# Optimization experiments

Measured on AMD Instinct MI355X. Metric: run time of the kernel, lower is better.

## Reference

```python
import jax, jax.numpy as jnp
import numpy as np

B, P, ENC = 64, 196, 512
EMB = ATT = DEC = 256
V = 10000
T = 44


def setup_inputs() -> dict:
    key = jax.random.key(0)
    ks = jax.random.split(key, 16)
    def xavier(k, shape):
        fan_out, fan_in = shape
        std = (2.0 / (fan_in + fan_out)) ** 0.5
        return jax.random.normal(k, shape, dtype=jnp.float32) * std
    return {
        "encoder_out": jax.random.normal(ks[0], (B, P, ENC), dtype=jnp.float32),
        "caption": jax.random.randint(ks[1], (B, T), 0, V),
        "W_enc_att": xavier(ks[2], (ATT, ENC)),
        "W_dec_att": xavier(ks[3], (ATT, DEC)),
        "W_full": xavier(ks[4], (1, ATT)),
        "embedding": jax.random.normal(ks[5], (V, EMB), dtype=jnp.float32) * 0.02,
        "W_init_h": xavier(ks[6], (DEC, ENC)),
        "b_init_h": jnp.zeros((DEC,), dtype=jnp.float32),
        "W_init_c": xavier(ks[7], (DEC, ENC)),
        "b_init_c": jnp.zeros((DEC,), dtype=jnp.float32),
        "W_ih": jax.random.normal(ks[8], (4 * DEC, EMB + ENC), dtype=jnp.float32) * 0.03,
        "b_ih": jnp.zeros((4 * DEC,), dtype=jnp.float32),
        "W_hh": jax.random.normal(ks[9], (4 * DEC, DEC), dtype=jnp.float32) * 0.03,
        "b_hh": jnp.zeros((4 * DEC,), dtype=jnp.float32),
        "W_out": xavier(ks[10], (V, DEC)),
        "b_out": jnp.zeros((V,), dtype=jnp.float32),
    }


def _decoder(encoder_out, caption, W_enc_att, W_dec_att, W_full, embedding,
             W_init_h, b_init_h, W_init_c, b_init_c,
             W_ih, b_ih, W_hh, b_hh, W_out, b_out):
    # embeddings: [B, T, EMB] -> time-major [T, B, EMB]
    emb = embedding[caption].transpose(1, 0, 2)
    # init hidden state from mean pooled encoder features
    avg = encoder_out.mean(axis=1)                      # [B, ENC]
    h0 = avg @ W_init_h.T + b_init_h                    # [B, DEC]
    c0 = avg @ W_init_c.T + b_init_c
    # attention key projection of encoder, constant over time
    att1 = jnp.einsum('bpe,ae->bpa', encoder_out, W_enc_att)  # [B, P, ATT]

    def step(carry, emb_t):
        h, c = carry
        # additive attention
        att2 = h @ W_dec_att.T                          # [B, ATT]
        scores = jnp.einsum('bpa,a->bp',
                            jax.nn.relu(att1 + att2[:, None, :]), W_full[0])
        alpha = jax.nn.softmax(scores, axis=1)          # [B, P]
        ctx = jnp.einsum('bp,bpe->be', alpha, encoder_out)  # [B, ENC]
        # LSTM cell (torch gate order: i, f, g, o)
        x = jnp.concatenate([ctx, emb_t], axis=1)       # [B, ENC+EMB]
        gates = x @ W_ih.T + b_ih + h @ W_hh.T + b_hh   # [B, 4*DEC]
        i, f, g, o = jnp.split(gates, 4, axis=1)
        c_new = jax.nn.sigmoid(f) * c + jax.nn.sigmoid(i) * jnp.tanh(g)
        h_new = jax.nn.sigmoid(o) * jnp.tanh(c_new)
        logits = h_new @ W_out.T + b_out                # [B, V]
        return (h_new, c_new), (logits, alpha)

    # NOTE: torch cat order is [weighted_context, embedding]
    (_, _), (logits, alphas) = jax.lax.scan(step, (h0, c0), emb)
    predictions = logits.transpose(1, 0, 2)             # [B, T, V]
    alphas = alphas.transpose(1, 0, 2)                  # [B, T, P]
    return predictions, alphas


def reference(encoder_out, caption, W_enc_att, W_dec_att, W_full, embedding,
              W_init_h, b_init_h, W_init_c, b_init_c,
              W_ih, b_ih, W_hh, b_hh, W_out, b_out):
    return _decoder(encoder_out, caption, W_enc_att, W_dec_att, W_full, embedding,
                    W_init_h, b_init_h, W_init_c, b_init_c,
                    W_ih, b_ih, W_hh, b_hh, W_out, b_out)
```

## Files before the change

kernel.cpp:

```cpp
#include <hip/hip_runtime.h>

#define B_   64
#define P_   196
#define ENC_ 512
#define ATT_ 256
#define DEC_ 256
#define EMB_ 256
#define V_   10000
#define T_   44
#define G4_  1024
#define XW_  768
#define A1N_ 26624

using short8 = __attribute__((ext_vector_type(8))) short;
using f32x4  = __attribute__((ext_vector_type(4))) float;
typedef _Float16 f16x2 __attribute__((ext_vector_type(2)));

__device__ __forceinline__ unsigned short f2bf(float f) {
    unsigned int u = __float_as_uint(f);
    unsigned int r = (u + 0x7fffu + ((u >> 16) & 1u)) >> 16;
    return (unsigned short)r;
}

__device__ __forceinline__ unsigned int pkh2(float a, float b) {
    f16x2 t; t.x = (_Float16)a; t.y = (_Float16)b;
    return __builtin_bit_cast(unsigned int, t);
}

__device__ __forceinline__ float fdot2f(float wbits, f16x2 xv, float acc) {
    f16x2 wv = __builtin_bit_cast(f16x2, wbits);
#if __has_builtin(__builtin_amdgcn_fdot2)
    return __builtin_amdgcn_fdot2(wv, xv, acc, false);
#else
    acc = fmaf((float)wv.x, (float)xv.x, acc);
    acc = fmaf((float)wv.y, (float)xv.y, acc);
    return acc;
#endif
}
__device__ __forceinline__ float fdot2u(unsigned int wbits, f16x2 xv, float acc) {
    f16x2 wv = __builtin_bit_cast(f16x2, wbits);
#if __has_builtin(__builtin_amdgcn_fdot2)
    return __builtin_amdgcn_fdot2(wv, xv, acc, false);
#else
    acc = fmaf((float)wv.x, (float)xv.x, acc);
    acc = fmaf((float)wv.y, (float)xv.y, acc);
    return acc;
#endif
}

__device__ __forceinline__ void bar() {
    asm volatile("s_waitcnt lgkmcnt(0)" ::: "memory");
    __builtin_amdgcn_s_barrier();
    asm volatile("" ::: "memory");
}

__global__ void k_transpose(const float* __restrict__ src, float* __restrict__ dst,
                            int N, int stride, int off) {
    __shared__ float t[32][33];
    int k0 = blockIdx.x * 32, n0 = blockIdx.y * 32;
    int tx = threadIdx.x & 31, ty = threadIdx.x >> 5;
    for (int r = ty; r < 32; r += 8)
        t[r][tx] = src[(size_t)(n0 + r) * stride + off + k0 + tx];
    __syncthreads();
    for (int r = ty; r < 32; r += 8)
        dst[(size_t)(k0 + r) * N + n0 + tx] = t[tx][r];
}

__global__ __launch_bounds__(256) void k_packWda(const float* __restrict__ Wda,
                                                 float4* __restrict__ WdaP4) {
    int d4 = blockIdx.x, a = threadIdx.x;
    float4 v;
    v.x = Wda[(size_t)a * DEC_ + 4 * d4 + 0];
    v.y = Wda[(size_t)a * DEC_ + 4 * d4 + 1];
    v.z = Wda[(size_t)a * DEC_ + 4 * d4 + 2];
    v.w = Wda[(size_t)a * DEC_ + 4 * d4 + 3];
    WdaP4[(size_t)d4 * 256 + a] = v;
}

__global__ __launch_bounds__(256) void k_packWg(const float* __restrict__ Wih,
        const float* __restrict__ Whh, float4* __restrict__ Wg4) {
    int k2 = blockIdx.x, d = threadIdx.x;
    int k = 2 * k2;
    unsigned int o[4];
#pragma unroll
    for (int g = 0; g < 4; ++g) {
        int row = g * 256 + d;
        float a0, a1;
        if (k < ENC_) {
            a0 = Wih[(size_t)row * XW_ + k];
            a1 = Wih[(size_t)row * XW_ + k + 1];
        } else {
            a0 = Whh[(size_t)row * DEC_ + k - ENC_];
            a1 = Whh[(size_t)row * DEC_ + k - ENC_ + 1];
        }
        o[g] = pkh2(a0, a1);
    }
    float4 v;
    v.x = __builtin_bit_cast(float, o[0]);
    v.y = __builtin_bit_cast(float, o[1]);
    v.z = __builtin_bit_cast(float, o[2]);
    v.w = __builtin_bit_cast(float, o[3]);
    Wg4[(size_t)k2 * 256 + d] = v;
}

__global__ __launch_bounds__(256) void k_packenc(const float* __restrict__ enc,
                                                 uint2* __restrict__ encPh) {
    int b = blockIdx.x, p4b = blockIdx.y * 7;
    for (int p4 = p4b; p4 < p4b + 7; ++p4) {
        for (int e = threadIdx.x; e < ENC_; e += 256) {
            float a0 = enc[((size_t)b * P_ + 4 * p4 + 0) * ENC_ + e];
            float a1 = enc[((size_t)b * P_ + 4 * p4 + 1) * ENC_ + e];
            float a2 = enc[((size_t)b * P_ + 4 * p4 + 2) * ENC_ + e];
            float a3 = enc[((size_t)b * P_ + 4 * p4 + 3) * ENC_ + e];
            uint2 v; v.x = pkh2(a0, a1); v.y = pkh2(a2, a3);
            encPh[((size_t)b * 49 + p4) * ENC_ + e] = v;
        }
    }
}

__global__ void k_cvt(const float* __restrict__ src, unsigned short* __restrict__ dst, int n) {
    int i = blockIdx.x * 256 + threadIdx.x;
    if (i < n) dst[i] = f2bf(src[i]);
}

__global__ __launch_bounds__(256) void k_init_state(
        const float* __restrict__ enc,
        const float* __restrict__ W_init_h, const float* __restrict__ b_init_h,
        const float* __restrict__ W_init_c, const float* __restrict__ b_init_c,
        float* __restrict__ h0, float* __restrict__ c0) {
    int b = blockIdx.x, tid = threadIdx.x;
    __shared__ float avg[ENC_];
    for (int e = tid; e < ENC_; e += 256) {
        float s = 0.f;
        const float* p = enc + (size_t)b * P_ * ENC_ + e;
        for (int i = 0; i < P_; i++) s += p[(size_t)i * ENC_];
        avg[e] = s * (1.0f / (float)P_);
    }
    __syncthreads();
    int d = tid;
    float hs = b_init_h[d], cs = b_init_c[d];
    const float* wh = W_init_h + (size_t)d * ENC_;
    const float* wc = W_init_c + (size_t)d * ENC_;
    for (int e = 0; e < ENC_; e++) { float a = avg[e]; hs += a * wh[e]; cs += a * wc[e]; }
    h0[b * DEC_ + d] = hs;
    c0[b * DEC_ + d] = cs;
}

__global__ __launch_bounds__(256) void k_att1(
        const float* __restrict__ enc, const float* __restrict__ Wea,
        unsigned int* __restrict__ att1h) {
    int b = blockIdx.x >> 2, a0 = (blockIdx.x & 3) * 64;
    __shared__ float encT[32][257];
    __shared__ float Wt[64][32];
    int tid = threadIdx.x;
    int pl = tid & 63, ia = tid >> 6;
    float acc[16][4];
#pragma unroll
    for (int k = 0; k < 16; k++)
#pragma unroll
        for (int qq = 0; qq < 4; qq++) acc[k][qq] = 0.f;

    for (int e0 = 0; e0 < ENC_; e0 += 32) {
        {
            int j = tid & 31, pr = tid >> 5;
            for (int pass = 0; pass < 32; pass++) {
                int p = pr + pass * 8;
                float v = 0.f;
                if (p < P_) v = enc[((size_t)b * P_ + p) * ENC_ + e0 + j];
                encT[j][p] = v;
            }
            int r = tid >> 2, c0 = (tid & 3) * 8;
#pragma unroll
            for (int i = 0; i < 8; i++)
                Wt[r][c0 + i] = Wea[(size_t)(a0 + r) * ENC_ + e0 + c0 + i];
        }
        __syncthreads();
        for (int e = 0; e < 32; e++) {
            float e0v = encT[e][pl], e1v = encT[e][pl + 64];
            float e2v = encT[e][pl + 128], e3v = encT[e][pl + 192];
#pragma unroll
            for (int k = 0; k < 16; k++) {
                float w = Wt[ia * 16 + k][e];
                acc[k][0] += w * e0v; acc[k][1] += w * e1v;
                acc[k][2] += w * e2v; acc[k][3] += w * e3v;
            }
        }
        __syncthreads();
    }
#pragma unroll
    for (int k = 0; k < 16; k += 2)
#pragma unroll
        for (int qq = 0; qq < 4; qq++) {
            int p = pl + 64 * qq;
            int a = a0 + ia * 16 + k;
            if (p < P_)
                att1h[(size_t)b * A1N_ + (size_t)(a >> 1) * 208 + p] =
                    pkh2(acc[k][qq], acc[k + 1][qq]);
        }
}

__global__ __launch_bounds__(256) void k_embW(
        const int* __restrict__ caption, const float* __restrict__ embedding,
        const float* __restrict__ WiheT, const float* __restrict__ b_ih,
        const float* __restrict__ b_hh, float* __restrict__ embW) {
    int r0 = blockIdx.x * 16, tid = threadIdx.x;
    __shared__ float embL[16][256];
    __shared__ int capL[16];
    if (tid < 16) {
        int r = r0 + tid, t = r >> 6, b = r & 63;
        capL[tid] = caption[b * T_ + t];
    }
    __syncthreads();
#pragma unroll
    for (int lr = 0; lr < 16; lr++)
        embL[lr][tid] = embedding[(size_t)capL[lr] * EMB_ + tid];
    __syncthreads();
    float base0 = b_ih[tid] + b_hh[tid];
    float base1 = b_ih[tid + 256] + b_hh[tid + 256];
    float base2 = b_ih[tid + 512] + b_hh[tid + 512];
    float base3 = b_ih[tid + 768] + b_hh[tid + 768];
    float acc[16][4];
#pragma unroll
    for (int lr = 0; lr < 16; lr++) {
        acc[lr][0] = base0; acc[lr][1] = base1; acc[lr][2] = base2; acc[lr][3] = base3;
    }
    for (int e = 0; e < EMB_; e++) {
        const float* wr = WiheT + (size_t)e * G4_ + tid;
        float w0 = wr[0], w1 = wr[256], w2 = wr[512], w3 = wr[768];
#pragma unroll
        for (int lr = 0; lr < 16; lr++) {
            float ev = embL[lr][e];
            acc[lr][0] += w0 * ev; acc[lr][1] += w1 * ev;
            acc[lr][2] += w2 * ev; acc[lr][3] += w3 * ev;
        }
    }
#pragma unroll
    for (int lr = 0; lr < 16; lr++) {
        float* o = embW + (size_t)(r0 + lr) * G4_ + tid;
        o[0] = acc[lr][0]; o[256] = acc[lr][1]; o[512] = acc[lr][2]; o[768] = acc[lr][3];
    }
}

__global__ __launch_bounds__(1024, 4) void k_recur(
        const unsigned int* __restrict__ att1h, const float4* __restrict__ WdaP4,
        const float* __restrict__ W_full, const float4* __restrict__ Wg4,
        const float* __restrict__ embW, const uint2* __restrict__ encPh,
        const float* __restrict__ h0, const float* __restrict__ c0,
        unsigned short* __restrict__ Hbf, float* __restrict__ out_alpha) {
    int b = blockIdx.x, tid = threadIdx.x;
    int q = tid >> 8;
    int r = tid & 255;
    int e5 = tid & 511, ph = tid >> 9;

    __shared__ __align__(16) float h_l[DEC_];
    __shared__ __align__(16) float att2_l[ATT_];
    __shared__ __align__(16) float wf_l[ATT_];
    __shared__ __align__(16) _Float16 xh[XW_];
    __shared__ float p1[4][256];
    __shared__ float p2[4][256];
    __shared__ float p3[2][512];
    __shared__ __align__(16) float4 p4s[4][256];
    __shared__ float red_l[4];
    __shared__ __align__(8) _Float16 alpha_h[208];
    __shared__ unsigned int att1_lds[A1N_ + 48];

    {
        const unsigned int* a1g = att1h + (size_t)b * A1N_;
        for (int i = tid; i < A1N_; i += 1024) att1_lds[i] = a1g[i];
    }
    if (tid < 256) {
        float hv = h0[b * DEC_ + tid];
        h_l[tid] = hv;
        xh[512 + tid] = (_Float16)hv;
        wf_l[tid] = W_full[tid];
    }
    float c = (tid < 256) ? c0[b * DEC_ + tid] : 0.f;
    __syncthreads();

    const uint2* encb = encPh + (size_t)b * (49 * ENC_);

    for (int t = 0; t < T_; ++t) {
        float a2 = 0.f;
#pragma unroll 4
        for (int i = 0; i < 16; i++) {
            int d4 = q * 16 + i;
            float4 w = WdaP4[(size_t)d4 * 256 + r];
            float4 h4 = *reinterpret_cast<const float4*>(&h_l[4 * d4]);
            a2 += w.x * h4.x + w.y * h4.y + w.z * h4.z + w.w * h4.w;
        }
        p1[q][r] = a2;
        bar();
        if (tid < 256) att2_l[tid] = p1[0][tid] + p1[1][tid] + p1[2][tid] + p1[3][tid];
        bar();

        float sp = 0.f;
#pragma unroll 4
        for (int i = 0; i < 32; i++) {
            int a2i = q * 32 + i;
            f16x2 av = __builtin_bit_cast(f16x2, att1_lds[a2i * 208 + r]);
            float2 t2 = *reinterpret_cast<const float2*>(&att2_l[2 * a2i]);
            float2 w4 = *reinterpret_cast<const float2*>(&wf_l[2 * a2i]);
            sp += fmaxf((float)av.x + t2.x, 0.f) * w4.x +
                  fmaxf((float)av.y + t2.y, 0.f) * w4.y;
        }
        p2[q][r] = sp;
        bar();

        float ex = 0.f;
        if (tid < 256) {
            float s = p2[0][tid] + p2[1][tid] + p2[2][tid] + p2[3][tid];
            ex = (tid < P_) ? __expf(s) : 0.f;
            float sm = ex;
#pragma unroll
            for (int off = 32; off; off >>= 1) sm += __shfl_xor(sm, off);
            if ((tid & 63) == 0) red_l[tid >> 6] = sm;
        }
        bar();
        if (tid < 256) {
            float sm = red_l[0] + red_l[1] + red_l[2] + red_l[3];
            float alpha = ex / sm;
            if (tid < 208) alpha_h[tid] = (_Float16)alpha;
            if (tid < P_) out_alpha[(size_t)b * (T_ * P_) + t * P_ + tid] = alpha;
        }
        bar();

        float cx = 0.f;
        {
            int p4b = ph ? 25 : 0, p4e = ph ? 49 : 25;
#pragma unroll 5
            for (int p4 = p4b; p4 < p4e; p4++) {
                uint2 ev = encb[(size_t)p4 * ENC_ + e5];
                f16x2 a01 = *reinterpret_cast<const f16x2*>(&alpha_h[4 * p4]);
                f16x2 a23 = *reinterpret_cast<const f16x2*>(&alpha_h[4 * p4 + 2]);
                cx = fdot2u(ev.x, a01, cx);
                cx = fdot2u(ev.y, a23, cx);
            }
        }
        p3[ph][e5] = cx;
        float ew0 = 0.f, ew1 = 0.f, ew2 = 0.f, ew3 = 0.f;
        if (tid < 256) {
            const float* ew = embW + ((size_t)t * B_ + b) * G4_;
            ew0 = ew[tid]; ew1 = ew[tid + 256]; ew2 = ew[tid + 512]; ew3 = ew[tid + 768];
        }
        bar();
        if (tid < 512) xh[tid] = (_Float16)(p3[0][tid] + p3[1][tid]);
        bar();

        float4 acc = {0.f, 0.f, 0.f, 0.f};
#pragma unroll 8
        for (int i = 0; i < 96; i++) {
            int k2 = q * 96 + i;
            float4 w = Wg4[(size_t)k2 * 256 + r];
            f16x2 xv = *reinterpret_cast<const f16x2*>(&xh[2 * k2]);
            acc.x = fdot2f(w.x, xv, acc.x);
            acc.y = fdot2f(w.y, xv, acc.y);
            acc.z = fdot2f(w.z, xv, acc.z);
            acc.w = fdot2f(w.w, xv, acc.w);
        }
        p4s[q][r] = acc;
        bar();

        if (tid < 256) {
            float4 g0 = p4s[0][tid], g1 = p4s[1][tid], g2 = p4s[2][tid], g3 = p4s[3][tid];
            float gi = g0.x + g1.x + g2.x + g3.x + ew0;
            float gf = g0.y + g1.y + g2.y + g3.y + ew1;
            float gg = g0.z + g1.z + g2.z + g3.z + ew2;
            float go = g0.w + g1.w + g2.w + g3.w + ew3;
            float i_g = 1.f / (1.f + __expf(-gi));
            float f_g = 1.f / (1.f + __expf(-gf));
            float g_g = tanhf(gg);
            float o_g = 1.f / (1.f + __expf(-go));
            c = f_g * c + i_g * g_g;
            float hn = o_g * tanhf(c);
            h_l[tid] = hn;
            xh[512 + tid] = (_Float16)hn;
            Hbf[((size_t)t * B_ + b) * DEC_ + tid] = f2bf(hn);
        }
        bar();
    }
}

__global__ __launch_bounds__(256) void k_logits(
        const unsigned short* __restrict__ Hbf, const unsigned short* __restrict__ Woutbf,
        const float* __restrict__ b_out, float* __restrict__ out) {
    int n0 = blockIdx.x * 128, m0 = blockIdx.y * 128;
    __shared__ __align__(16) unsigned short At[128][40];
    __shared__ __align__(16) unsigned short Bt[128][40];
    int tid = threadIdx.x;
    int lane = tid & 63, w = tid >> 6;
    int wm = (w & 1) * 64, wn = (w >> 1) * 64;
    f32x4 acc[4][4];
#pragma unroll
    for (int i = 0; i < 4; i++)
#pragma unroll
        for (int j = 0; j < 4; j++) acc[i][j] = (f32x4){0.f, 0.f, 0.f, 0.f};

    for (int k0 = 0; k0 < DEC_; k0 += 32) {
#pragma unroll
        for (int l = 0; l < 2; l++) {
            int idx = l * 256 + tid;
            int r = idx >> 2, kc = (idx & 3) * 8;
            uint4 av = *reinterpret_cast<const uint4*>(&Hbf[(size_t)(m0 + r) * DEC_ + k0 + kc]);
            *reinterpret_cast<uint4*>(&At[r][kc]) = av;
            uint4 bv = make_uint4(0u, 0u, 0u, 0u);
            if (n0 + r < V_)
                bv = *reinterpret_cast<const uint4*>(&Woutbf[(size_t)(n0 + r) * DEC_ + k0 + kc]);
            *reinterpret_cast<uint4*>(&Bt[r][kc]) = bv;
        }
        __syncthreads();
        int qk = (lane >> 4) * 8, fr = lane & 15;
        short8 a[4], bb[4];
#pragma unroll
        for (int i = 0; i < 4; i++) {
            a[i]  = *reinterpret_cast<const short8*>(&At[wm + i * 16 + fr][qk]);
            bb[i] = *reinterpret_cast<const short8*>(&Bt[wn + i * 16 + fr][qk]);
        }
#pragma unroll
        for (int i = 0; i < 4; i++)
#pragma unroll
            for (int j = 0; j < 4; j++)
                acc[i][j] = __builtin_amdgcn_mfma_f32_16x16x32_bf16(a[i], bb[j], acc[i][j], 0, 0, 0);
        __syncthreads();
    }
    int col = lane & 15, qr = (lane >> 4) * 4;
#pragma unroll
    for (int j = 0; j < 4; j++) {
        int n = n0 + wn + j * 16 + col;
        if (n < V_) {
            float bo = b_out[n];
#pragma unroll
            for (int i = 0; i < 4; i++)
#pragma unroll
                for (int rr = 0; rr < 4; rr++) {
                    int m = m0 + wm + i * 16 + qr + rr;
                    int t = m >> 6, bb2 = m & 63;
                    out[(size_t)bb2 * (T_ * V_) + (size_t)t * V_ + n] = acc[i][j][rr] + bo;
                }
        }
    }
}

extern "C" void kernel_launch(void* const* d_in, const int* in_sizes, int n_in,
                              void* d_out, int out_size, void* d_ws, size_t ws_size,
                              hipStream_t stream) {
    const float* enc       = (const float*)d_in[0];
    const int*   caption   = (const int*)d_in[1];
    const float* W_enc_att = (const float*)d_in[2];
    const float* W_dec_att = (const float*)d_in[3];
    const float* W_full    = (const float*)d_in[4];
    const float* embedding = (const float*)d_in[5];
    const float* W_init_h  = (const float*)d_in[6];
    const float* b_init_h  = (const float*)d_in[7];
    const float* W_init_c  = (const float*)d_in[8];
    const float* b_init_c  = (const float*)d_in[9];
    const float* W_ih      = (const float*)d_in[10];
    const float* b_ih      = (const float*)d_in[11];
    const float* W_hh      = (const float*)d_in[12];
    const float* b_hh      = (const float*)d_in[13];
    const float* W_out     = (const float*)d_in[14];
    const float* b_out     = (const float*)d_in[15];

    float* ws = (float*)d_ws;
    float* h0    = ws;
    float* c0    = ws + 16384;
    float* WdaP  = ws + 32768;
    float* WiheT = ws + 98304;
    float* Wg4   = ws + 360448;
    float* embW  = ws + 753664;
    float* att1h = ws + 3637248;
    float* encPh = ws + 5341184;
    unsigned short* Hbf    = (unsigned short*)(ws + 8552448);
    unsigned short* Woutbf = (unsigned short*)(ws + 8912896);

    float* out_pred  = (float*)d_out;
    float* out_alpha = out_pred + (size_t)B_ * T_ * V_;

    k_transpose<<<dim3(8, 32), 256, 0, stream>>>(W_ih, WiheT, G4_, XW_, ENC_);
    k_packWda<<<64, 256, 0, stream>>>(W_dec_att, (float4*)WdaP);
    k_packWg<<<384, 256, 0, stream>>>(W_ih, W_hh, (float4*)Wg4);
    k_packenc<<<dim3(64, 7), 256, 0, stream>>>(enc, (uint2*)encPh);
    k_cvt<<<10000, 256, 0, stream>>>(W_out, Woutbf, V_ * DEC_);
    k_init_state<<<B_, 256, 0, stream>>>(enc, W_init_h, b_init_h, W_init_c, b_init_c, h0, c0);
    k_att1<<<B_ * 4, 256, 0, stream>>>(enc, W_enc_att, (unsigned int*)att1h);
    k_embW<<<176, 256, 0, stream>>>(caption, embedding, WiheT, b_ih, b_hh, embW);
    k_recur<<<B_, 1024, 0, stream>>>((const unsigned int*)att1h, (const float4*)WdaP, W_full,
                                     (const float4*)Wg4, embW, (const uint2*)encPh,
                                     h0, c0, Hbf, out_alpha);
    k_logits<<<dim3(79, 22), 256, 0, stream>>>(Hbf, Woutbf, b_out, out_pred);
}
```

Measured before the change: 1.414 ms.

## Precompute encoder×W_ih projection so recurrence contracts alpha against projected features

Uses linearity to rewrite ctx@W_ih_ctx^T as alpha-weighted sum of a precomputed per-batch enc@W_ih_ctx^T table, computed once by a new MFMA GEMM kernel. The recurrence then only needs two concurrent reductions, over 196 pixels of projected features and over 256 hidden units of W_hh, which removes the serial context-then-gate GEMM and one barrier stage. att1 is also moved from LDS into per-thread registers. The cost is a larger per-batch table (196×1024 fp16) streamed from global memory each step and higher register pressure.

```diff
diff --git a/kernel.cpp b/kernel.cpp
--- a/kernel.cpp
+++ b/kernel.cpp
@@ -11,8 +11,10 @@
 #define G4_  1024
 #define XW_  768
 #define A1N_ 26624
+#define EWR_ 98
 
 using short8 = __attribute__((ext_vector_type(8))) short;
+using half8  = __attribute__((ext_vector_type(8))) _Float16;
 using f32x4  = __attribute__((ext_vector_type(4))) float;
 typedef _Float16 f16x2 __attribute__((ext_vector_type(2)));
 
@@ -27,16 +29,6 @@
     return __builtin_bit_cast(unsigned int, t);
 }
 
-__device__ __forceinline__ float fdot2f(float wbits, f16x2 xv, float acc) {
-    f16x2 wv = __builtin_bit_cast(f16x2, wbits);
-#if __has_builtin(__builtin_amdgcn_fdot2)
-    return __builtin_amdgcn_fdot2(wv, xv, acc, false);
-#else
-    acc = fmaf((float)wv.x, (float)xv.x, acc);
-    acc = fmaf((float)wv.y, (float)xv.y, acc);
-    return acc;
-#endif
-}
 __device__ __forceinline__ float fdot2u(unsigned int wbits, f16x2 xv, float acc) {
     f16x2 wv = __builtin_bit_cast(f16x2, wbits);
 #if __has_builtin(__builtin_amdgcn_fdot2)
@@ -77,43 +69,79 @@
     WdaP4[(size_t)d4 * 256 + a] = v;
 }
 
-__global__ __launch_bounds__(256) void k_packWg(const float* __restrict__ Wih,
-        const float* __restrict__ Whh, float4* __restrict__ Wg4) {
-    int k2 = blockIdx.x, d = threadIdx.x;
-    int k = 2 * k2;
-    unsigned int o[4];
-#pragma unroll
-    for (int g = 0; g < 4; ++g) {
-        int row = g * 256 + d;
-        float a0, a1;
-        if (k < ENC_) {
-            a0 = Wih[(size_t)row * XW_ + k];
-            a1 = Wih[(size_t)row * XW_ + k + 1];
-        } else {
-            a0 = Whh[(size_t)row * DEC_ + k - ENC_];
-            a1 = Whh[(size_t)row * DEC_ + k - ENC_ + 1];
-        }
-        o[g] = pkh2(a0, a1);
-    }
-    float4 v;
-    v.x = __builtin_bit_cast(float, o[0]);
-    v.y = __builtin_bit_cast(float, o[1]);
-    v.z = __builtin_bit_cast(float, o[2]);
-    v.w = __builtin_bit_cast(float, o[3]);
-    Wg4[(size_t)k2 * 256 + d] = v;
-}
-
-__global__ __launch_bounds__(256) void k_packenc(const float* __restrict__ enc,
-                                                 uint2* __restrict__ encPh) {
-    int b = blockIdx.x, p4b = blockIdx.y * 7;
-    for (int p4 = p4b; p4 < p4b + 7; ++p4) {
-        for (int e = threadIdx.x; e < ENC_; e += 256) {
-            float a0 = enc[((size_t)b * P_ + 4 * p4 + 0) * ENC_ + e];
-            float a1 = enc[((size_t)b * P_ + 4 * p4 + 1) * ENC_ + e];
-            float a2 = enc[((size_t)b * P_ + 4 * p4 + 2) * ENC_ + e];
-            float a3 = enc[((size_t)b * P_ + 4 * p4 + 3) * ENC_ + e];
-            uint2 v; v.x = pkh2(a0, a1); v.y = pkh2(a2, a3);
-            encPh[((size_t)b * 49 + p4) * ENC_ + e] = v;
+__global__ __launch_bounds__(256) void k_packWhh(const float* __restrict__ Whh,
+                                                 unsigned int* __restrict__ WhhP) {
+    int d2 = blockIdx.x;
+    int j = blockIdx.y * 256 + threadIdx.x;
+    WhhP[(size_t)d2 * 1024 + j] =
+        pkh2(Whh[(size_t)j * DEC_ + 2 * d2], Whh[(size_t)j * DEC_ + 2 * d2 + 1]);
+}
+
+__global__ __launch_bounds__(256) void k_encW(
+        const float* __restrict__ enc, const float* __restrict__ Wih,
+        unsigned int* __restrict__ encW) {
+    int n0 = blockIdx.x * 128, m0 = blockIdx.y * 128, b = blockIdx.z;
+    __shared__ __align__(16) unsigned short At[128][40];
+    __shared__ __align__(16) unsigned short Bt[128][40];
+    int tid = threadIdx.x;
+    int lane = tid & 63, w = tid >> 6;
+    int wm = (w & 1) * 64, wn = (w >> 1) * 64;
+    f32x4 acc[4][4];
+#pragma unroll
+    for (int i = 0; i < 4; i++)
+#pragma unroll
+        for (int j = 0; j < 4; j++) acc[i][j] = (f32x4){0.f, 0.f, 0.f, 0.f};
+
+    for (int k0 = 0; k0 < ENC_; k0 += 32) {
+#pragma unroll
+        for (int l = 0; l < 2; l++) {
+            int idx = l * 256 + tid;
+            int r = idx >> 2, kcf = (idx & 3) * 8;
+            uint4 av = make_uint4(0u, 0u, 0u, 0u);
+            int p = m0 + r;
+            if (p < P_) {
+                const float* ap = enc + ((size_t)b * P_ + p) * ENC_ + k0 + kcf;
+                float4 f0 = *reinterpret_cast<const float4*>(ap);
+                float4 f1 = *reinterpret_cast<const float4*>(ap + 4);
+                av.x = pkh2(f0.x, f0.y); av.y = pkh2(f0.z, f0.w);
+                av.z = pkh2(f1.x, f1.y); av.w = pkh2(f1.z, f1.w);
+            }
+            *reinterpret_cast<uint4*>(&At[r][kcf]) = av;
+            const float* bp = Wih + (size_t)(n0 + r) * XW_ + k0 + kcf;
+            float4 g0 = *reinterpret_cast<const float4*>(bp);
+            float4 g1 = *reinterpret_cast<const float4*>(bp + 4);
+            uint4 bv;
+            bv.x = pkh2(g0.x, g0.y); bv.y = pkh2(g0.z, g0.w);
+            bv.z = pkh2(g1.x, g1.y); bv.w = pkh2(g1.z, g1.w);
+            *reinterpret_cast<uint4*>(&Bt[r][kcf]) = bv;
+        }
+        __syncthreads();
+        int qk = (lane >> 4) * 8, fr = lane & 15;
+        half8 a[4], bb[4];
+#pragma unroll
+        for (int i = 0; i < 4; i++) {
+            a[i]  = *reinterpret_cast<const half8*>(&At[wm + i * 16 + fr][qk]);
+            bb[i] = *reinterpret_cast<const half8*>(&Bt[wn + i * 16 + fr][qk]);
+        }
+#pragma unroll
+        for (int i = 0; i < 4; i++)
+#pragma unroll
+            for (int j = 0; j < 4; j++)
+                acc[i][j] = __builtin_amdgcn_mfma_f32_16x16x32_f16(a[i], bb[j], acc[i][j], 0, 0, 0);
+        __syncthreads();
+    }
+    unsigned int* eb = encW + (size_t)b * (EWR_ * 1024);
+    int col = lane & 15, qr = (lane >> 4) * 4;
+#pragma unroll
+    for (int j = 0; j < 4; j++) {
+        int n = n0 + wn + j * 16 + col;
+#pragma unroll
+        for (int i = 0; i < 4; i++) {
+            int row0 = m0 + wm + i * 16 + qr;
+            if (row0 < P_)
+                eb[(size_t)(row0 >> 1) * 1024 + n] = pkh2(acc[i][j][0], acc[i][j][1]);
+            if (row0 + 2 < P_)
+                eb[(size_t)((row0 >> 1) + 1) * 1024 + n] = pkh2(acc[i][j][2], acc[i][j][3]);
         }
     }
 }
@@ -243,41 +271,48 @@
 
 __global__ __launch_bounds__(1024, 4) void k_recur(
         const unsigned int* __restrict__ att1h, const float4* __restrict__ WdaP4,
-        const float* __restrict__ W_full, const float4* __restrict__ Wg4,
-        const float* __restrict__ embW, const uint2* __restrict__ encPh,
+        const float* __restrict__ W_full, const unsigned int* __restrict__ WhhP,
+        const unsigned int* __restrict__ encW, const float* __restrict__ embW,
         const float* __restrict__ h0, const float* __restrict__ c0,
         unsigned short* __restrict__ Hbf, float* __restrict__ out_alpha) {
     int b = blockIdx.x, tid = threadIdx.x;
     int q = tid >> 8;
     int r = tid & 255;
-    int e5 = tid & 511, ph = tid >> 9;
+    int j4 = tid & 255;
+    int sub = (tid >> 8) & 1;
+    bool isW = tid >= 512;
 
     __shared__ __align__(16) float h_l[DEC_];
     __shared__ __align__(16) float att2_l[ATT_];
     __shared__ __align__(16) float wf_l[ATT_];
-    __shared__ __align__(16) _Float16 xh[XW_];
+    __shared__ __align__(4) _Float16 hh_h[DEC_];
+    __shared__ __align__(4) _Float16 alpha_h[212];
     __shared__ float p1[4][256];
     __shared__ float p2[4][256];
-    __shared__ float p3[2][512];
-    __shared__ __align__(16) float4 p4s[4][256];
+    __shared__ __align__(16) float4 pj[2][256];
+    __shared__ __align__(16) float4 pw[2][256];
+    __shared__ float gl[G4_];
     __shared__ float red_l[4];
-    __shared__ __align__(8) _Float16 alpha_h[208];
-    __shared__ unsigned int att1_lds[A1N_ + 48];
-
+
+    unsigned int a1r[32];
     {
-        const unsigned int* a1g = att1h + (size_t)b * A1N_;
-        for (int i = tid; i < A1N_; i += 1024) att1_lds[i] = a1g[i];
+        int rc = (r < 208) ? r : 207;
+        const unsigned int* a1g = att1h + (size_t)b * A1N_ + (size_t)(q * 32) * 208 + rc;
+#pragma unroll
+        for (int i = 0; i < 32; i++) a1r[i] = a1g[(size_t)i * 208];
     }
     if (tid < 256) {
         float hv = h0[b * DEC_ + tid];
         h_l[tid] = hv;
-        xh[512 + tid] = (_Float16)hv;
+        hh_h[tid] = (_Float16)hv;
         wf_l[tid] = W_full[tid];
     }
+    if (tid < 212) alpha_h[tid] = (_Float16)0.f;
     float c = (tid < 256) ? c0[b * DEC_ + tid] : 0.f;
     __syncthreads();
 
-    const uint2* encb = encPh + (size_t)b * (49 * ENC_);
+    const uint4* encW4 = reinterpret_cast<const uint4*>(encW + (size_t)b * (EWR_ * 1024));
+    const uint4* whh4  = reinterpret_cast<const uint4*>(WhhP);
 
     for (int t = 0; t < T_; ++t) {
         float a2 = 0.f;
@@ -294,10 +329,10 @@
         bar();
 
         float sp = 0.f;
-#pragma unroll 4
+#pragma unroll
         for (int i = 0; i < 32; i++) {
             int a2i = q * 32 + i;
-            f16x2 av = __builtin_bit_cast(f16x2, att1_lds[a2i * 208 + r]);
+            f16x2 av = __builtin_bit_cast(f16x2, a1r[i]);
             float2 t2 = *reinterpret_cast<const float2*>(&att2_l[2 * a2i]);
             float2 w4 = *reinterpret_cast<const float2*>(&wf_l[2 * a2i]);
             sp += fmaxf((float)av.x + t2.x, 0.f) * w4.x +
@@ -322,50 +357,48 @@
             if (tid < 208) alpha_h[tid] = (_Float16)alpha;
             if (tid < P_) out_alpha[(size_t)b * (T_ * P_) + t * P_ + tid] = alpha;
         }
-        bar();
-
-        float cx = 0.f;
+        float ewj = embW[((size_t)t * B_ + b) * G4_ + tid];
+        bar();
+
+        float4 acc = {0.f, 0.f, 0.f, 0.f};
+        if (!isW) {
+            int p2b = sub * 49;
+#pragma unroll 7
+            for (int i = 0; i < 49; i++) {
+                int pp = p2b + i;
+                uint4 w = encW4[(size_t)pp * 256 + j4];
+                f16x2 al = *reinterpret_cast<const f16x2*>(&alpha_h[2 * pp]);
+                acc.x = fdot2u(w.x, al, acc.x);
+                acc.y = fdot2u(w.y, al, acc.y);
+                acc.z = fdot2u(w.z, al, acc.z);
+                acc.w = fdot2u(w.w, al, acc.w);
+            }
+            pj[sub][j4] = acc;
+        } else {
+            int d2b = sub * 64;
+#pragma unroll 8
+            for (int i = 0; i < 64; i++) {
+                int dd = d2b + i;
+                uint4 w = whh4[(size_t)dd * 256 + j4];
+                f16x2 h2v = *reinterpret_cast<const f16x2*>(&hh_h[2 * dd]);
+                acc.x = fdot2u(w.x, h2v, acc.x);
+                acc.y = fdot2u(w.y, h2v, acc.y);
+                acc.z = fdot2u(w.z, h2v, acc.z);
+                acc.w = fdot2u(w.w, h2v, acc.w);
+            }
+            pw[sub][j4] = acc;
+        }
+        bar();
+
         {
-            int p4b = ph ? 25 : 0, p4e = ph ? 49 : 25;
-#pragma unroll 5
-            for (int p4 = p4b; p4 < p4e; p4++) {
-                uint2 ev = encb[(size_t)p4 * ENC_ + e5];
-                f16x2 a01 = *reinterpret_cast<const f16x2*>(&alpha_h[4 * p4]);
-                f16x2 a23 = *reinterpret_cast<const f16x2*>(&alpha_h[4 * p4 + 2]);
-                cx = fdot2u(ev.x, a01, cx);
-                cx = fdot2u(ev.y, a23, cx);
-            }
-        }
-        p3[ph][e5] = cx;
-        float ew0 = 0.f, ew1 = 0.f, ew2 = 0.f, ew3 = 0.f;
+            const float* pjF = reinterpret_cast<const float*>(pj);
+            const float* pwF = reinterpret_cast<const float*>(pw);
+            gl[tid] = pjF[tid] + pjF[1024 + tid] + pwF[tid] + pwF[1024 + tid] + ewj;
+        }
+        bar();
+
         if (tid < 256) {
-            const float* ew = embW + ((size_t)t * B_ + b) * G4_;
-            ew0 = ew[tid]; ew1 = ew[tid + 256]; ew2 = ew[tid + 512]; ew3 = ew[tid + 768];
-        }
-        bar();
-        if (tid < 512) xh[tid] = (_Float16)(p3[0][tid] + p3[1][tid]);
-        bar();
-
-        float4 acc = {0.f, 0.f, 0.f, 0.f};
-#pragma unroll 8
-        for (int i = 0; i < 96; i++) {
-            int k2 = q * 96 + i;
-            float4 w = Wg4[(size_t)k2 * 256 + r];
-            f16x2 xv = *reinterpret_cast<const f16x2*>(&xh[2 * k2]);
-            acc.x = fdot2f(w.x, xv, acc.x);
-            acc.y = fdot2f(w.y, xv, acc.y);
-            acc.z = fdot2f(w.z, xv, acc.z);
-            acc.w = fdot2f(w.w, xv, acc.w);
-        }
-        p4s[q][r] = acc;
-        bar();
-
-        if (tid < 256) {
-            float4 g0 = p4s[0][tid], g1 = p4s[1][tid], g2 = p4s[2][tid], g3 = p4s[3][tid];
-            float gi = g0.x + g1.x + g2.x + g3.x + ew0;
-            float gf = g0.y + g1.y + g2.y + g3.y + ew1;
-            float gg = g0.z + g1.z + g2.z + g3.z + ew2;
-            float go = g0.w + g1.w + g2.w + g3.w + ew3;
+            float gi = gl[tid], gf = gl[tid + 256], gg = gl[tid + 512], go = gl[tid + 768];
             float i_g = 1.f / (1.f + __expf(-gi));
             float f_g = 1.f / (1.f + __expf(-gf));
             float g_g = tanhf(gg);
@@ -373,7 +406,7 @@
             c = f_g * c + i_g * g_g;
             float hn = o_g * tanhf(c);
             h_l[tid] = hn;
-            xh[512 + tid] = (_Float16)hn;
+            hh_h[tid] = (_Float16)hn;
             Hbf[((size_t)t * B_ + b) * DEC_ + tid] = f2bf(hn);
         }
         bar();
@@ -465,26 +498,26 @@
     float* c0    = ws + 16384;
     float* WdaP  = ws + 32768;
     float* WiheT = ws + 98304;
-    float* Wg4   = ws + 360448;
-    float* embW  = ws + 753664;
-    float* att1h = ws + 3637248;
-    float* encPh = ws + 5341184;
-    unsigned short* Hbf    = (unsigned short*)(ws + 8552448);
-    unsigned short* Woutbf = (unsigned short*)(ws + 8912896);
+    float* WhhP  = ws + 360448;
+    float* embW  = ws + 491520;
+    float* att1h = ws + 3375104;
+    float* encW  = ws + 5079040;
+    unsigned short* Hbf    = (unsigned short*)(ws + 11501568);
+    unsigned short* Woutbf = (unsigned short*)(ws + 11862016);
 
     float* out_pred  = (float*)d_out;
     float* out_alpha = out_pred + (size_t)B_ * T_ * V_;
 
     k_transpose<<<dim3(8, 32), 256, 0, stream>>>(W_ih, WiheT, G4_, XW_, ENC_);
     k_packWda<<<64, 256, 0, stream>>>(W_dec_att, (float4*)WdaP);
-    k_packWg<<<384, 256, 0, stream>>>(W_ih, W_hh, (float4*)Wg4);
-    k_packenc<<<dim3(64, 7), 256, 0, stream>>>(enc, (uint2*)encPh);
+    k_packWhh<<<dim3(128, 4), 256, 0, stream>>>(W_hh, (unsigned int*)WhhP);
+    k_encW<<<dim3(8, 2, 64), 256, 0, stream>>>(enc, W_ih, (unsigned int*)encW);
     k_cvt<<<10000, 256, 0, stream>>>(W_out, Woutbf, V_ * DEC_);
     k_init_state<<<B_, 256, 0, stream>>>(enc, W_init_h, b_init_h, W_init_c, b_init_c, h0, c0);
     k_att1<<<B_ * 4, 256, 0, stream>>>(enc, W_enc_att, (unsigned int*)att1h);
     k_embW<<<176, 256, 0, stream>>>(caption, embedding, WiheT, b_ih, b_hh, embW);
     k_recur<<<B_, 1024, 0, stream>>>((const unsigned int*)att1h, (const float4*)WdaP, W_full,
-                                     (const float4*)Wg4, embW, (const uint2*)encPh,
-                                     h0, c0, Hbf, out_alpha);
+                                     (const unsigned int*)WhhP, (const unsigned int*)encW,
+                                     embW, h0, c0, Hbf, out_alpha);
     k_logits<<<dim3(79, 22), 256, 0, stream>>>(Hbf, Woutbf, b_out, out_pred);
 }
```

Result: slower. 1.695 ms (+19.8%).
